# Optimization experiments

Measured on AMD Instinct MI355X. Metric: run time of the kernel, lower is better.

## Reference

```python
import jax, jax.numpy as jnp
import numpy as np

H, KV, D, HID, FF = 32, 8, 128, 4096, 14336
EPS = 1e-5
ROPE_THETA = 1e9


def setup_inputs() -> dict:
    key = jax.random.key(0)
    ks = jax.random.split(key, 10)
    B, S = 1, 2048
    s = 0.02
    return {
        "hidden_states": jax.random.normal(ks[0], (B, S, HID), dtype=jnp.float32),
        "wq": jax.random.normal(ks[1], (HID, H * D), dtype=jnp.float32) * s,
        "wk": jax.random.normal(ks[2], (HID, KV * D), dtype=jnp.float32) * s,
        "wv": jax.random.normal(ks[3], (HID, KV * D), dtype=jnp.float32) * s,
        "wo": jax.random.normal(ks[4], (H * D, HID), dtype=jnp.float32) * s,
        "w_gate": jax.random.normal(ks[5], (HID, FF), dtype=jnp.float32) * s,
        "w_up": jax.random.normal(ks[6], (HID, FF), dtype=jnp.float32) * s,
        "w_down": jax.random.normal(ks[7], (FF, HID), dtype=jnp.float32) * s,
        "ln1_w": jnp.ones((HID,), dtype=jnp.float32),
        "ln2_w": jnp.ones((HID,), dtype=jnp.float32),
        "position_ids": jnp.arange(B * S, dtype=jnp.int32).reshape(B, S),
    }


def _rmsnorm(x, w):
    var = jnp.mean(jnp.square(x), axis=-1, keepdims=True)
    return x * jax.lax.rsqrt(var + EPS) * w


def _rope_cos_sin(position_ids):
    inv_freq = 1.0 / (ROPE_THETA ** (jnp.arange(0, D, 2, dtype=jnp.float32) / D))  # [D/2]
    ang = position_ids.astype(jnp.float32)[..., None] * inv_freq  # [B,S,D/2]
    ang = jnp.concatenate([ang, ang], axis=-1)  # [B,S,D]
    return jnp.cos(ang), jnp.sin(ang)


def _rotate_half(x):
    x1, x2 = x[..., : D // 2], x[..., D // 2:]
    return jnp.concatenate([-x2, x1], axis=-1)


def _apply_rope(x, cos, sin):
    # x: [B,S,h,D]; cos/sin: [B,S,D]
    c, s = cos[:, :, None, :], sin[:, :, None, :]
    return x * c + _rotate_half(x) * s


def reference(hidden_states, wq, wk, wv, wo, w_gate, w_up, w_down, ln1_w, ln2_w, position_ids):
    B, S, _ = hidden_states.shape
    G = H // KV  # query groups per kv head

    # --- attention block ---
    residual = hidden_states
    x = _rmsnorm(hidden_states, ln1_w)
    q = (x @ wq).reshape(B, S, H, D)
    k = (x @ wk).reshape(B, S, KV, D)
    v = (x @ wv).reshape(B, S, KV, D)

    cos, sin = _rope_cos_sin(position_ids)
    q = _apply_rope(q, cos, sin)
    k = _apply_rope(k, cos, sin)

    # GQA: group query heads over kv heads, [B,S,KV,G,D]
    qg = q.reshape(B, S, KV, G, D)
    scores = jnp.einsum("bqhgd,bkhd->bhgqk", qg, k) / jnp.sqrt(jnp.float32(D))
    causal = position_ids[:, :, None] >= position_ids[:, None, :]  # [B,S,S]
    scores = jnp.where(causal[:, None, None, :, :], scores, jnp.float32(-1e9))
    probs = jax.nn.softmax(scores, axis=-1)
    attn = jnp.einsum("bhgqk,bkhd->bqhgd", probs, v).reshape(B, S, H * D)
    hidden_states = residual + attn @ wo

    # --- MLP block (SwiGLU) ---
    residual = hidden_states
    x = _rmsnorm(hidden_states, ln2_w)
    mlp = (jax.nn.silu(x @ w_gate) * (x @ w_up)) @ w_down
    return residual + mlp
```

## Files before the change

kernel.cpp:

```cpp
#include <hip/hip_runtime.h>

typedef short bf16x8 __attribute__((ext_vector_type(8)));
typedef float f32x4 __attribute__((ext_vector_type(4)));

#define DEV __device__ __forceinline__

constexpr int SEQ = 2048;
constexpr int HID = 4096;
constexpr int NH  = 32;
constexpr int NKV = 8;
constexpr int DH  = 128;
constexpr int FF  = 14336;
constexpr int QKVN = NH * DH + 2 * NKV * DH;

DEV unsigned short f2bf(float f) {
  union { float f; unsigned u; } x; x.f = f;
  unsigned r = x.u + 0x7fffu + ((x.u >> 16) & 1u);
  return (unsigned short)(r >> 16);
}
DEV float bf2f(unsigned short u) {
  union { unsigned u; float f; } x; x.u = ((unsigned)u) << 16; return x.f;
}
DEV void gload16(const void* g, void* l) {
  __builtin_amdgcn_global_load_lds(
      (const __attribute__((address_space(1))) unsigned*)g,
      (__attribute__((address_space(3))) unsigned*)l, 16, 0, 0);
}

__global__ __launch_bounds__(256) void rmsnorm_kernel(
    const float* __restrict__ x, const float* __restrict__ w,
    unsigned short* __restrict__ out) {
  const int row = blockIdx.x;
  const int tid = threadIdx.x;
  const float* xr = x + (size_t)row * HID;
  float4 v[4];
  float ss = 0.f;
#pragma unroll
  for (int i = 0; i < 4; ++i) {
    v[i] = *(const float4*)(xr + i * 1024 + tid * 4);
    ss += v[i].x * v[i].x + v[i].y * v[i].y + v[i].z * v[i].z + v[i].w * v[i].w;
  }
#pragma unroll
  for (int m = 1; m < 64; m <<= 1) ss += __shfl_xor(ss, m);
  __shared__ float red[4];
  if ((tid & 63) == 0) red[tid >> 6] = ss;
  __syncthreads();
  float tot = red[0] + red[1] + red[2] + red[3];
  float rms = rsqrtf(tot / (float)HID + 1e-5f);
  unsigned short* orow = out + (size_t)row * HID;
#pragma unroll
  for (int i = 0; i < 4; ++i) {
    int base = i * 1024 + tid * 4;
    ushort4 o;
    o.x = f2bf(v[i].x * rms * w[base + 0]);
    o.y = f2bf(v[i].y * rms * w[base + 1]);
    o.z = f2bf(v[i].z * rms * w[base + 2]);
    o.w = f2bf(v[i].w * rms * w[base + 3]);
    *(ushort4*)(orow + base) = o;
  }
}

__global__ __launch_bounds__(256) void wtrans_kernel(
    const float* __restrict__ W, unsigned short* __restrict__ WT, int K,
    int N) {
  __shared__ unsigned short t[64][72];
  const int k0 = blockIdx.x * 64, n0 = blockIdx.y * 64;
  const int tid = threadIdx.x;
  const int tk = tid >> 4;
  const int tn4 = (tid & 15) * 4;
#pragma unroll
  for (int p = 0; p < 4; ++p) {
    int k = tk + p * 16;
    float4 v = *(const float4*)(W + (size_t)(k0 + k) * N + n0 + tn4);
    t[tn4 + 0][k] = f2bf(v.x);
    t[tn4 + 1][k] = f2bf(v.y);
    t[tn4 + 2][k] = f2bf(v.z);
    t[tn4 + 3][k] = f2bf(v.w);
  }
  __syncthreads();
#pragma unroll
  for (int p = 0; p < 4; ++p) {
    int n = tk + p * 16;
    ushort4 o = *(const ushort4*)&t[n][tn4];
    *(ushort4*)(WT + (size_t)(n0 + n) * K + k0 + tn4) = o;
  }
}

__global__ __launch_bounds__(256) void rope_kernel(unsigned short* __restrict__ x,
                                                   int nheads, int ld) {
  const int gid = blockIdx.x * 256 + threadIdx.x;
  const int i = gid & 63;
  const int t = gid >> 6;
  const int s = t / nheads;
  const int hh = t - s * nheads;
  float ang = (float)s * exp2f((float)i * (-29.897352853986263f / 64.f));
  float sn, cs;
  sincosf(ang, &sn, &cs);
  size_t base = (size_t)s * ld + hh * DH + i;
  float x1 = bf2f(x[base]);
  float x2 = bf2f(x[base + 64]);
  x[base]      = f2bf(x1 * cs - x2 * sn);
  x[base + 64] = f2bf(x2 * cs + x1 * sn);
}

__global__ __launch_bounds__(256) void silu_mul_kernel(
    const unsigned short* __restrict__ g, const unsigned short* __restrict__ u,
    unsigned short* __restrict__ out) {
  const size_t idx = ((size_t)blockIdx.x * 256 + threadIdx.x) * 4;
  ushort4 gv = *(const ushort4*)(g + idx);
  ushort4 uv = *(const ushort4*)(u + idx);
  float gf[4] = {bf2f(gv.x), bf2f(gv.y), bf2f(gv.z), bf2f(gv.w)};
  float uf[4] = {bf2f(uv.x), bf2f(uv.y), bf2f(uv.z), bf2f(uv.w)};
  ushort4 o;
  unsigned short* op = (unsigned short*)&o;
#pragma unroll
  for (int j = 0; j < 4; ++j) {
    float sl = gf[j] / (1.f + __expf(-gf[j]));
    op[j] = f2bf(sl * uf[j]);
  }
  *(ushort4*)(out + idx) = o;
}

__global__ __launch_bounds__(256) void combine_kernel(
    const float* __restrict__ p0, const float* __restrict__ p1,
    const float* __restrict__ res, float* __restrict__ out) {
  const size_t i = ((size_t)blockIdx.x * 256 + threadIdx.x) * 4;
  float4 a = *(const float4*)(p0 + i);
  float4 b = *(const float4*)(p1 + i);
  float4 c = *(const float4*)(res + i);
  float4 o;
  o.x = a.x + b.x + c.x;
  o.y = a.y + b.y + c.y;
  o.z = a.z + b.z + c.z;
  o.w = a.w + b.w + c.w;
  *(float4*)(out + i) = o;
}

template <int EPI>
__global__ __launch_bounds__(512, 2) void gemm8p_kernel(
    const unsigned short* __restrict__ A, const unsigned short* __restrict__ BT,
    void* __restrict__ Cv0, void* __restrict__ Cv1, int gridM, int N, int Kld,
    int nsplit) {
  constexpr int MF = 4;
  constexpr int ABYTES = 256 * 128;
  constexpr int BUFBYTES = ABYTES + 32768;
  __shared__ __align__(128) char sm[2 * BUFBYTES];

  const int tid  = threadIdx.x;
  const int lane = tid & 63;
  const int wv   = tid >> 6;
  const int nwg = gridDim.x;
  const int b = blockIdx.x;
  const int logical = (b & 7) * (nwg >> 3) + (b >> 3);
  const int ntiles = nwg / nsplit;
  const int s = logical / ntiles;
  const int r = logical - s * ntiles;
  const int m0 = (r % gridM) * 256;
  const int n0 = (r / gridM) * 256;
  const int Klen = Kld / nsplit;
  const int koff = s * Klen;
  const int wm = (wv >> 2) * 128;
  const int wn = (wv & 3) * 64;
  const int nt = Klen >> 6;

  const int srow = tid >> 3;
  const int scolb = (tid & 7) * 16;
  const int sldsbase = wv * 1024;

  auto stage = [&](int h, int t) {
    const int buf = t & 1;
    const int kt = koff + t * 64;
    char* ldsOp;
    const unsigned short* g;
    int grow0, rowBase;
    if (h < 2) {
      ldsOp = sm + buf * BUFBYTES + ABYTES; g = BT; grow0 = n0; rowBase = h * 128;
    } else {
      ldsOp = sm + buf * BUFBYTES;          g = A;  grow0 = m0; rowBase = (h - 2) * 128;
    }
#pragma unroll
    for (int rr = 0; rr < 2; ++rr) {
      int row = rowBase + rr * 64 + srow;
      const char* gp = (const char*)g + ((size_t)(grow0 + row) * Kld + kt) * 2 +
                       (scolb ^ ((row & 7) << 4));
      gload16(gp, ldsOp + rowBase * 128 + rr * 8192 + sldsbase);
    }
  };

  const int kb0 = (lane >> 4) * 16;
  const int lrow = lane & 15;
  auto ldA = [&](const char* sA, int mh, int mf, int ks) {
    int row = wm + mh * 64 + mf * 16 + lrow;
    return *(const bf16x8*)(sA + ((row * 128 + kb0 + ks * 64) ^ ((row & 7) << 4)));
  };
  auto ldB = [&](const char* sB, int j, int ks) {
    int col = wn + j * 16 + lrow;
    return *(const bf16x8*)(sB + ((col * 128 + kb0 + ks * 64) ^ ((col & 7) << 4)));
  };

  f32x4 acc[2 * MF][4] = {};

  stage(2, 0); stage(3, 0); stage(0, 0); stage(1, 0);
  if (nt > 1) {
    stage(0, 1); stage(1, 1);
    asm volatile("s_waitcnt vmcnt(4)" ::: "memory");
  } else {
    asm volatile("s_waitcnt vmcnt(0)" ::: "memory");
  }
  __builtin_amdgcn_s_barrier();

  for (int t = 0; t < nt; ++t) {
    const char* sA = sm + (t & 1) * BUFBYTES;
    const char* sB = sA + ABYTES;
    bf16x8 a[MF], bb[4][2];

#pragma unroll
    for (int j = 0; j < 4; ++j) bb[j][0] = ldB(sB, j, 0);
#pragma unroll
    for (int mf = 0; mf < MF; ++mf) a[mf] = ldA(sA, 0, mf, 0);
    if (t + 1 < nt) stage(2, t + 1);
    __builtin_amdgcn_sched_barrier(0);
    __builtin_amdgcn_s_barrier();
    __builtin_amdgcn_s_setprio(1);
#pragma unroll
    for (int mf = 0; mf < MF; ++mf)
#pragma unroll
      for (int j = 0; j < 4; ++j)
        acc[mf][j] = __builtin_amdgcn_mfma_f32_16x16x32_bf16(
            a[mf], bb[j][0], acc[mf][j], 0, 0, 0);
    __builtin_amdgcn_s_setprio(0);
    __builtin_amdgcn_sched_barrier(0);
    __builtin_amdgcn_s_barrier();

#pragma unroll
    for (int j = 0; j < 4; ++j) bb[j][1] = ldB(sB, j, 1);
#pragma unroll
    for (int mf = 0; mf < MF; ++mf) a[mf] = ldA(sA, 0, mf, 1);
    if (t + 1 < nt) stage(3, t + 1);
    __builtin_amdgcn_sched_barrier(0);
    __builtin_amdgcn_s_barrier();
    __builtin_amdgcn_s_setprio(1);
#pragma unroll
    for (int mf = 0; mf < MF; ++mf)
#pragma unroll
      for (int j = 0; j < 4; ++j)
        acc[mf][j] = __builtin_amdgcn_mfma_f32_16x16x32_bf16(
            a[mf], bb[j][1], acc[mf][j], 0, 0, 0);
    __builtin_amdgcn_s_setprio(0);
    __builtin_amdgcn_sched_barrier(0);
    __builtin_amdgcn_s_barrier();

#pragma unroll
    for (int mf = 0; mf < MF; ++mf) a[mf] = ldA(sA, 1, mf, 0);
    if (t + 2 < nt) stage(0, t + 2);
    __builtin_amdgcn_sched_barrier(0);
    __builtin_amdgcn_s_barrier();
    __builtin_amdgcn_s_setprio(1);
#pragma unroll
    for (int mf = 0; mf < MF; ++mf)
#pragma unroll
      for (int j = 0; j < 4; ++j)
        acc[MF + mf][j] = __builtin_amdgcn_mfma_f32_16x16x32_bf16(
            a[mf], bb[j][0], acc[MF + mf][j], 0, 0, 0);
    __builtin_amdgcn_s_setprio(0);
    __builtin_amdgcn_sched_barrier(0);
    __builtin_amdgcn_s_barrier();

#pragma unroll
    for (int mf = 0; mf < MF; ++mf) a[mf] = ldA(sA, 1, mf, 1);
    if (t + 2 < nt) {
      stage(1, t + 2);
      asm volatile("s_waitcnt vmcnt(4)" ::: "memory");
    } else {
      asm volatile("s_waitcnt vmcnt(0)" ::: "memory");
    }
    __builtin_amdgcn_sched_barrier(0);
    __builtin_amdgcn_s_barrier();
    __builtin_amdgcn_s_setprio(1);
#pragma unroll
    for (int mf = 0; mf < MF; ++mf)
#pragma unroll
      for (int j = 0; j < 4; ++j)
        acc[MF + mf][j] = __builtin_amdgcn_mfma_f32_16x16x32_bf16(
            a[mf], bb[j][1], acc[MF + mf][j], 0, 0, 0);
    __builtin_amdgcn_s_setprio(0);
    __builtin_amdgcn_sched_barrier(0);
    __builtin_amdgcn_s_barrier();
  }

  const int rb = (lane >> 4) * 4;
  float* P = (float*)(s ? Cv1 : Cv0);
#pragma unroll
  for (int i = 0; i < 2 * MF; ++i) {
    const int mh = i / MF, mf = i % MF;
#pragma unroll
    for (int j = 0; j < 4; ++j) {
#pragma unroll
      for (int rr = 0; rr < 4; ++rr) {
        size_t row = (size_t)(m0 + wm + mh * 64 + mf * 16 + rb + rr);
        size_t col = (size_t)(n0 + wn + j * 16 + lrow);
        float vv = acc[i][j][rr];
        if (EPI == 0) {
          ((unsigned short*)Cv0)[row * N + col] = f2bf(vv);
        } else {
          P[row * N + col] = vv;
        }
      }
    }
  }
}

__global__ __launch_bounds__(512, 1) void attn_kernel(
    const unsigned short* __restrict__ QKV, unsigned short* __restrict__ Ob) {
  __shared__ __align__(128) char sm[114688];
  char* sQ  = sm;
  char* sK0 = sm + 32768;
  char* sK1 = sm + 49152;
  char* sV0 = sm + 65536;
  char* sV1 = sm + 81920;
  char* sP  = sm + 98304;
  const int tid  = threadIdx.x;
  const int lane = tid & 63;
  const int wv   = tid >> 6;
  const int logical = blockIdx.x;
  const int xr = 15 - (logical >> 5);
  const int h = logical & 31;
  const int qb0 = xr * 128;
  const int hkv = h >> 2;
  const int rbase = (lane >> 4) * 4;
  const int cbase = lane & 15;
  const unsigned short* Qp = QKV + h * DH;
  const unsigned short* Kp = QKV + NH * DH + hkv * DH;
  const unsigned short* Vp = QKV + NH * DH + NKV * DH + hkv * DH;

#pragma unroll
  for (int i = 0; i < 4; ++i) {
    int offs = i * 8192 + tid * 16;
    int row = offs >> 8, col = offs & 255;
    const char* gp = (const char*)Qp + ((size_t)(qb0 + row) * QKVN) * 2 +
                     (col ^ ((row & 15) << 4));
    gload16(gp, sQ + i * 8192 + wv * 1024);
  }

  auto stageK = [&](int t) {
    char* dst = (t & 1) ? sK1 : sK0;
    const int kt0 = t * 64;
#pragma unroll
    for (int i = 0; i < 2; ++i) {
      int offs = i * 8192 + tid * 16;
      int row = offs >> 8, col = offs & 255;
      const char* gp = (const char*)Kp + ((size_t)(kt0 + row) * QKVN) * 2 +
                       (col ^ ((row & 15) << 4));
      gload16(gp, dst + i * 8192 + wv * 1024);
    }
  };

  const int d4  = (tid & 31) * 4;
  const int kv4 = (tid >> 5) * 4;
  const int rot = (tid >> 1) & 3;
  auto loadV = [&](int t, ushort4* vr) {
    const unsigned short* g0 = Vp + (size_t)(t * 64 + kv4) * QKVN + d4;
#pragma unroll
    for (int k = 0; k < 4; ++k) vr[k] = *(const ushort4*)(g0 + (size_t)k * QKVN);
  };
  auto writeV = [&](int t, const ushort4* vr) {
    char* dst = (t & 1) ? sV1 : sV0;
    const unsigned short* a0 = (const unsigned short*)&vr[0];
    const unsigned short* a1 = (const unsigned short*)&vr[1];
    const unsigned short* a2 = (const unsigned short*)&vr[2];
    const unsigned short* a3 = (const unsigned short*)&vr[3];
#pragma unroll
    for (int j = 0; j < 4; ++j) {
      int jj = (j + rot) & 3;
      int dd = d4 + jj;
      uint2 pk;
      pk.x = (unsigned)a0[jj] | ((unsigned)a1[jj] << 16);
      pk.y = (unsigned)a2[jj] | ((unsigned)a3[jj] << 16);
      *(uint2*)(dst + ((dd * 128 + kv4 * 2) ^ ((dd & 7) << 4))) = pk;
    }
  };

  ushort4 vr[4];
  stageK(0);
  loadV(0, vr);
  asm volatile("s_waitcnt vmcnt(0)" ::: "memory");
  writeV(0, vr);
  __syncthreads();

  const int qrow = wv * 16 + (lane & 15);
  bf16x8 aq[4];
#pragma unroll
  for (int kk = 0; kk < 4; ++kk) {
    int kb = (lane >> 4) * 16 + kk * 64;
    aq[kk] = *(const bf16x8*)(sQ + ((qrow * 256 + kb) ^ ((qrow & 15) << 4)));
  }

  f32x4 oacc[8] = {};
  float m_r[4] = {-1e30f, -1e30f, -1e30f, -1e30f};
  float l_r[4] = {0.f, 0.f, 0.f, 0.f};
  const int ntiles = 2 * (xr + 1);

  for (int t = 0; t < ntiles; ++t) {
    const int kt0 = t * 64;
    const char* cK = (t & 1) ? sK1 : sK0;
    const char* cV = (t & 1) ? sV1 : sV0;
    if (t + 1 < ntiles) {
      stageK(t + 1);
      loadV(t + 1, vr);
    }

    f32x4 sacc[4] = {};
#pragma unroll
    for (int kk = 0; kk < 4; ++kk) {
      int kb = (lane >> 4) * 16 + kk * 64;
#pragma unroll
      for (int ni = 0; ni < 4; ++ni) {
        int krow = ni * 16 + (lane & 15);
        bf16x8 bk =
            *(const bf16x8*)(cK + ((krow * 256 + kb) ^ ((krow & 15) << 4)));
        sacc[ni] = __builtin_amdgcn_mfma_f32_16x16x32_bf16(aq[kk], bk,
                                                           sacc[ni], 0, 0, 0);
      }
    }

    const float scale = 0.08838834764831845f;
#pragma unroll
    for (int r = 0; r < 4; ++r) {
      int qg = qb0 + wv * 16 + rbase + r;
      float mx = -1e30f;
#pragma unroll
      for (int ni = 0; ni < 4; ++ni) {
        int cg = kt0 + ni * 16 + cbase;
        float sv = sacc[ni][r] * scale;
        sv = (cg <= qg) ? sv : -1e30f;
        sacc[ni][r] = sv;
        mx = fmaxf(mx, sv);
      }
      mx = fmaxf(mx, __shfl_xor(mx, 1));
      mx = fmaxf(mx, __shfl_xor(mx, 2));
      mx = fmaxf(mx, __shfl_xor(mx, 4));
      mx = fmaxf(mx, __shfl_xor(mx, 8));
      float mnew = fmaxf(m_r[r], mx);
      float sf = __expf(m_r[r] - mnew);
      m_r[r] = mnew;
      float rsum = 0.f;
#pragma unroll
      for (int ni = 0; ni < 4; ++ni) {
        float pv = __expf(sacc[ni][r] - mnew);
        sacc[ni][r] = pv;
        rsum += pv;
      }
      rsum += __shfl_xor(rsum, 1);
      rsum += __shfl_xor(rsum, 2);
      rsum += __shfl_xor(rsum, 4);
      rsum += __shfl_xor(rsum, 8);
      l_r[r] = l_r[r] * sf + rsum;
#pragma unroll
      for (int nt2 = 0; nt2 < 8; ++nt2) oacc[nt2][r] *= sf;
    }

    char* pw = sP + wv * 2048;
#pragma unroll
    for (int ni = 0; ni < 4; ++ni)
#pragma unroll
      for (int r = 0; r < 4; ++r) {
        int row = rbase + r;
        int cb2 = (ni * 16 + cbase) * 2;
        *(unsigned short*)(pw + ((row * 128 + cb2) ^ ((row & 7) << 4))) =
            f2bf(sacc[ni][r]);
      }
    asm volatile("s_waitcnt lgkmcnt(0)" ::: "memory");

#pragma unroll
    for (int kk = 0; kk < 2; ++kk) {
      int kb = (lane >> 4) * 16 + kk * 64;
      int prow = lane & 15;
      bf16x8 ap =
          *(const bf16x8*)(pw + ((prow * 128 + kb) ^ ((prow & 7) << 4)));
#pragma unroll
      for (int nt2 = 0; nt2 < 8; ++nt2) {
        int vrow = nt2 * 16 + (lane & 15);
        bf16x8 bv =
            *(const bf16x8*)(cV + ((vrow * 128 + kb) ^ ((vrow & 7) << 4)));
        oacc[nt2] =
            __builtin_amdgcn_mfma_f32_16x16x32_bf16(ap, bv, oacc[nt2], 0, 0, 0);
      }
    }

    if (t + 1 < ntiles) {
      asm volatile("s_waitcnt vmcnt(0)" ::: "memory");
      writeV(t + 1, vr);
    }
    __syncthreads();
  }

#pragma unroll
  for (int nt2 = 0; nt2 < 8; ++nt2)
#pragma unroll
    for (int r = 0; r < 4; ++r) {
      size_t row = (size_t)(qb0 + wv * 16 + rbase + r);
      int col = nt2 * 16 + cbase;
      Ob[row * (NH * DH) + h * DH + col] = f2bf(oacc[nt2][r] / l_r[r]);
    }
}

extern "C" void kernel_launch(void* const* d_in, const int* in_sizes, int n_in,
                              void* d_out, int out_size, void* d_ws,
                              size_t ws_size, hipStream_t stream) {
  const float* hs  = (const float*)d_in[0];
  const float* wq  = (const float*)d_in[1];
  const float* wk  = (const float*)d_in[2];
  const float* wvp = (const float*)d_in[3];
  const float* wo  = (const float*)d_in[4];
  const float* wg  = (const float*)d_in[5];
  const float* wu  = (const float*)d_in[6];
  const float* wd  = (const float*)d_in[7];
  const float* ln1 = (const float*)d_in[8];
  const float* ln2 = (const float*)d_in[9];

  char* p = (char*)d_ws;
  size_t need = 0;
  auto alloc = [&](size_t bytes) {
    char* r = p + need;
    need += (bytes + 255) & ~(size_t)255;
    return r;
  };
  unsigned short* T1   = (unsigned short*)alloc((size_t)FF * HID * 2);
  unsigned short* xn   = (unsigned short*)alloc((size_t)SEQ * HID * 2);
  unsigned short* qkv  = (unsigned short*)alloc((size_t)SEQ * QKVN * 2);
  unsigned short* ab   = (unsigned short*)alloc((size_t)SEQ * NH * DH * 2);
  float*          h2   = (float*)alloc((size_t)SEQ * HID * 4);
  unsigned short* xn2  = (unsigned short*)alloc((size_t)SEQ * HID * 2);
  unsigned short* gbuf = (unsigned short*)alloc((size_t)SEQ * FF * 2);
  unsigned short* ubuf = (unsigned short*)alloc((size_t)SEQ * FF * 2);
  if (need > ws_size) return;

  float* pO0 = (float*)gbuf;
  float* pO1 = (float*)ubuf;
  float* pD0 = (float*)ubuf;
  float* pD1 = (float*)xn;

  rmsnorm_kernel<<<SEQ, 256, 0, stream>>>(hs, ln1, xn);
  wtrans_kernel<<<dim3(HID / 64, HID / 64), 256, 0, stream>>>(wq, T1, HID, HID);
  wtrans_kernel<<<dim3(HID / 64, (NKV * DH) / 64), 256, 0, stream>>>(
      wk, T1 + (size_t)(NH * DH) * HID, HID, NKV * DH);
  wtrans_kernel<<<dim3(HID / 64, (NKV * DH) / 64), 256, 0, stream>>>(
      wvp, T1 + (size_t)(NH * DH + NKV * DH) * HID, HID, NKV * DH);
  gemm8p_kernel<0><<<(SEQ / 256) * (QKVN / 256), 512, 0, stream>>>(
      xn, T1, qkv, nullptr, SEQ / 256, QKVN, HID, 1);
  rope_kernel<<<(SEQ * NH * 64) / 256, 256, 0, stream>>>(qkv, NH, QKVN);
  rope_kernel<<<(SEQ * NKV * 64) / 256, 256, 0, stream>>>(qkv + NH * DH, NKV,
                                                          QKVN);
  attn_kernel<<<512, 512, 0, stream>>>(qkv, ab);
  wtrans_kernel<<<dim3(HID / 64, HID / 64), 256, 0, stream>>>(wo, T1, HID, HID);
  gemm8p_kernel<2><<<(SEQ / 256) * (HID / 256) * 2, 512, 0, stream>>>(
      ab, T1, pO0, pO1, SEQ / 256, HID, HID, 2);
  combine_kernel<<<(SEQ * HID) / 1024, 256, 0, stream>>>(pO0, pO1, hs, h2);
  rmsnorm_kernel<<<SEQ, 256, 0, stream>>>(h2, ln2, xn2);
  wtrans_kernel<<<dim3(HID / 64, FF / 64), 256, 0, stream>>>(wg, T1, HID, FF);
  gemm8p_kernel<0><<<(SEQ / 256) * (FF / 256), 512, 0, stream>>>(
      xn2, T1, gbuf, nullptr, SEQ / 256, FF, HID, 1);
  wtrans_kernel<<<dim3(HID / 64, FF / 64), 256, 0, stream>>>(wu, T1, HID, FF);
  gemm8p_kernel<0><<<(SEQ / 256) * (FF / 256), 512, 0, stream>>>(
      xn2, T1, ubuf, nullptr, SEQ / 256, FF, HID, 1);
  silu_mul_kernel<<<((size_t)SEQ * FF) / 1024, 256, 0, stream>>>(gbuf, ubuf,
                                                                 gbuf);
  wtrans_kernel<<<dim3(FF / 64, HID / 64), 256, 0, stream>>>(wd, T1, FF, HID);
  gemm8p_kernel<2><<<(SEQ / 256) * (HID / 256) * 2, 512, 0, stream>>>(
      gbuf, T1, pD0, pD1, SEQ / 256, HID, FF, 2);
  combine_kernel<<<(SEQ * HID) / 1024, 256, 0, stream>>>(pD0, pD1, h2,
                                                         (float*)d_out);
}
```

Measured before the change: 1.318 ms.

## Overlap weight transposes with GEMMs, fuse SiLU-mul into up GEMM and combine with RMSNorm

Adds extra workgroups to the GEMM kernel that transpose and convert the next weight matrix into a second buffer while the GEMM tiles run, so the Wo, Wup and Wdown transposes overlap compute instead of running as separate launches. The SiLU-multiply is fused into the up-projection epilogue, which reads the gate output in place and removes the ubuf round trip and the separate elementwise kernel. The attention-output combine is fused with the second RMSNorm. This path needs a larger workspace (the fat path) and falls back to the serial schedule otherwise. The transpose blocks compete with GEMM blocks for CUs and bandwidth, and the gate-input read in the epilogue adds uncoalesced loads.

```diff
diff --git a/kernel.cpp b/kernel.cpp
--- a/kernel.cpp
+++ b/kernel.cpp
@@ -103,24 +103,6 @@
   x[base + 64] = f2bf(x2 * cs + x1 * sn);
 }
 
-__global__ __launch_bounds__(256) void silu_mul_kernel(
-    const unsigned short* __restrict__ g, const unsigned short* __restrict__ u,
-    unsigned short* __restrict__ out) {
-  const size_t idx = ((size_t)blockIdx.x * 256 + threadIdx.x) * 4;
-  ushort4 gv = *(const ushort4*)(g + idx);
-  ushort4 uv = *(const ushort4*)(u + idx);
-  float gf[4] = {bf2f(gv.x), bf2f(gv.y), bf2f(gv.z), bf2f(gv.w)};
-  float uf[4] = {bf2f(uv.x), bf2f(uv.y), bf2f(uv.z), bf2f(uv.w)};
-  ushort4 o;
-  unsigned short* op = (unsigned short*)&o;
-#pragma unroll
-  for (int j = 0; j < 4; ++j) {
-    float sl = gf[j] / (1.f + __expf(-gf[j]));
-    op[j] = f2bf(sl * uf[j]);
-  }
-  *(ushort4*)(out + idx) = o;
-}
-
 __global__ __launch_bounds__(256) void combine_kernel(
     const float* __restrict__ p0, const float* __restrict__ p1,
     const float* __restrict__ res, float* __restrict__ out) {
@@ -136,20 +118,95 @@
   *(float4*)(out + i) = o;
 }
 
+__global__ __launch_bounds__(256) void combine_rms_kernel(
+    const float* __restrict__ p0, const float* __restrict__ p1,
+    const float* __restrict__ res, const float* __restrict__ w,
+    float* __restrict__ h2, unsigned short* __restrict__ xn2) {
+  const int row = blockIdx.x;
+  const int tid = threadIdx.x;
+  const size_t base = (size_t)row * HID;
+  float4 h[4];
+  float ss = 0.f;
+#pragma unroll
+  for (int i = 0; i < 4; ++i) {
+    size_t idx = base + i * 1024 + tid * 4;
+    float4 a = *(const float4*)(p0 + idx);
+    float4 b = *(const float4*)(p1 + idx);
+    float4 c = *(const float4*)(res + idx);
+    h[i].x = a.x + b.x + c.x;
+    h[i].y = a.y + b.y + c.y;
+    h[i].z = a.z + b.z + c.z;
+    h[i].w = a.w + b.w + c.w;
+    *(float4*)(h2 + idx) = h[i];
+    ss += h[i].x * h[i].x + h[i].y * h[i].y + h[i].z * h[i].z + h[i].w * h[i].w;
+  }
+#pragma unroll
+  for (int m = 1; m < 64; m <<= 1) ss += __shfl_xor(ss, m);
+  __shared__ float red[4];
+  if ((tid & 63) == 0) red[tid >> 6] = ss;
+  __syncthreads();
+  float tot = red[0] + red[1] + red[2] + red[3];
+  float rms = rsqrtf(tot / (float)HID + 1e-5f);
+#pragma unroll
+  for (int i = 0; i < 4; ++i) {
+    int off = i * 1024 + tid * 4;
+    ushort4 o;
+    o.x = f2bf(h[i].x * rms * w[off + 0]);
+    o.y = f2bf(h[i].y * rms * w[off + 1]);
+    o.z = f2bf(h[i].z * rms * w[off + 2]);
+    o.w = f2bf(h[i].w * rms * w[off + 3]);
+    *(ushort4*)(xn2 + base + off) = o;
+  }
+}
+
 template <int EPI>
 __global__ __launch_bounds__(512, 2) void gemm8p_kernel(
     const unsigned short* __restrict__ A, const unsigned short* __restrict__ BT,
     void* __restrict__ Cv0, void* __restrict__ Cv1, int gridM, int N, int Kld,
-    int nsplit) {
+    int nsplit, const float* __restrict__ TW, unsigned short* __restrict__ TWT,
+    int TK, int TN, int n_t) {
   constexpr int MF = 4;
   constexpr int ABYTES = 256 * 128;
   constexpr int BUFBYTES = ABYTES + 32768;
   __shared__ __align__(128) char sm[2 * BUFBYTES];
 
-  const int tid  = threadIdx.x;
+  const int tid = threadIdx.x;
+  const int nwg = gridDim.x - n_t;
+
+  if ((int)blockIdx.x >= nwg) {
+    const int team = tid >> 8, lt = tid & 255;
+    unsigned short(*tt)[72] = (unsigned short(*)[72])(sm + team * 9216);
+    const int tilesK = TK >> 6;
+    const int tot = tilesK * (TN >> 6);
+    const int tk = lt >> 4;
+    const int tn4 = (lt & 15) * 4;
+    for (int tile = ((int)blockIdx.x - nwg) * 2 + team; tile < tot;
+         tile += n_t * 2) {
+      const int k0 = (tile % tilesK) << 6;
+      const int n0t = (tile / tilesK) << 6;
+#pragma unroll
+      for (int p = 0; p < 4; ++p) {
+        int k = tk + p * 16;
+        float4 v = *(const float4*)(TW + (size_t)(k0 + k) * TN + n0t + tn4);
+        tt[tn4 + 0][k] = f2bf(v.x);
+        tt[tn4 + 1][k] = f2bf(v.y);
+        tt[tn4 + 2][k] = f2bf(v.z);
+        tt[tn4 + 3][k] = f2bf(v.w);
+      }
+      __syncthreads();
+#pragma unroll
+      for (int p = 0; p < 4; ++p) {
+        int n = tk + p * 16;
+        ushort4 o = *(const ushort4*)&tt[n][tn4];
+        *(ushort4*)(TWT + (size_t)(n0t + n) * TK + k0 + tn4) = o;
+      }
+      __syncthreads();
+    }
+    return;
+  }
+
   const int lane = tid & 63;
   const int wv   = tid >> 6;
-  const int nwg = gridDim.x;
   const int b = blockIdx.x;
   const int logical = (b & 7) * (nwg >> 3) + (b >> 3);
   const int ntiles = nwg / nsplit;
@@ -302,8 +359,12 @@
         float vv = acc[i][j][rr];
         if (EPI == 0) {
           ((unsigned short*)Cv0)[row * N + col] = f2bf(vv);
+        } else if (EPI == 2) {
+          P[row * N + col] = vv;
         } else {
-          P[row * N + col] = vv;
+          float g = bf2f(((const unsigned short*)Cv1)[row * N + col]);
+          float sl = g / (1.f + __expf(-g));
+          ((unsigned short*)Cv0)[row * N + col] = f2bf(sl * vv);
         }
       }
     }
@@ -533,12 +594,16 @@
   unsigned short* xn2  = (unsigned short*)alloc((size_t)SEQ * HID * 2);
   unsigned short* gbuf = (unsigned short*)alloc((size_t)SEQ * FF * 2);
   unsigned short* ubuf = (unsigned short*)alloc((size_t)SEQ * FF * 2);
-  if (need > ws_size) return;
+  size_t need_base = need;
+  unsigned short* T2   = (unsigned short*)alloc((size_t)FF * HID * 2);
+  const bool fat = (ws_size >= need);
+  if (ws_size < need_base) return;
 
   float* pO0 = (float*)gbuf;
-  float* pO1 = (float*)ubuf;
-  float* pD0 = (float*)ubuf;
-  float* pD1 = (float*)xn;
+  float* pO1 = (float*)xn;
+  float* pD0 = fat ? (float*)T2 : (float*)ubuf;
+  float* pD1 = fat ? (float*)(T2 + (size_t)SEQ * HID * 2) : (float*)xn;
+  (void)ubuf;
 
   rmsnorm_kernel<<<SEQ, 256, 0, stream>>>(hs, ln1, xn);
   wtrans_kernel<<<dim3(HID / 64, HID / 64), 256, 0, stream>>>(wq, T1, HID, HID);
@@ -546,28 +611,43 @@
       wk, T1 + (size_t)(NH * DH) * HID, HID, NKV * DH);
   wtrans_kernel<<<dim3(HID / 64, (NKV * DH) / 64), 256, 0, stream>>>(
       wvp, T1 + (size_t)(NH * DH + NKV * DH) * HID, HID, NKV * DH);
-  gemm8p_kernel<0><<<(SEQ / 256) * (QKVN / 256), 512, 0, stream>>>(
-      xn, T1, qkv, nullptr, SEQ / 256, QKVN, HID, 1);
+  if (fat) {
+    gemm8p_kernel<0><<<192 + 64, 512, 0, stream>>>(
+        xn, T1, qkv, nullptr, SEQ / 256, QKVN, HID, 1, wo, T2, HID, HID, 64);
+  } else {
+    gemm8p_kernel<0><<<192, 512, 0, stream>>>(
+        xn, T1, qkv, nullptr, SEQ / 256, QKVN, HID, 1, nullptr, nullptr, 64, 64, 0);
+  }
   rope_kernel<<<(SEQ * NH * 64) / 256, 256, 0, stream>>>(qkv, NH, QKVN);
   rope_kernel<<<(SEQ * NKV * 64) / 256, 256, 0, stream>>>(qkv + NH * DH, NKV,
                                                           QKVN);
   attn_kernel<<<512, 512, 0, stream>>>(qkv, ab);
-  wtrans_kernel<<<dim3(HID / 64, HID / 64), 256, 0, stream>>>(wo, T1, HID, HID);
-  gemm8p_kernel<2><<<(SEQ / 256) * (HID / 256) * 2, 512, 0, stream>>>(
-      ab, T1, pO0, pO1, SEQ / 256, HID, HID, 2);
-  combine_kernel<<<(SEQ * HID) / 1024, 256, 0, stream>>>(pO0, pO1, hs, h2);
-  rmsnorm_kernel<<<SEQ, 256, 0, stream>>>(h2, ln2, xn2);
+  unsigned short* Wo = fat ? T2 : T1;
+  if (!fat)
+    wtrans_kernel<<<dim3(HID / 64, HID / 64), 256, 0, stream>>>(wo, T1, HID, HID);
+  gemm8p_kernel<2><<<256, 512, 0, stream>>>(
+      ab, Wo, pO0, pO1, SEQ / 256, HID, HID, 2, nullptr, nullptr, 64, 64, 0);
+  combine_rms_kernel<<<SEQ, 256, 0, stream>>>(pO0, pO1, hs, ln2, h2, xn2);
   wtrans_kernel<<<dim3(HID / 64, FF / 64), 256, 0, stream>>>(wg, T1, HID, FF);
-  gemm8p_kernel<0><<<(SEQ / 256) * (FF / 256), 512, 0, stream>>>(
-      xn2, T1, gbuf, nullptr, SEQ / 256, FF, HID, 1);
-  wtrans_kernel<<<dim3(HID / 64, FF / 64), 256, 0, stream>>>(wu, T1, HID, FF);
-  gemm8p_kernel<0><<<(SEQ / 256) * (FF / 256), 512, 0, stream>>>(
-      xn2, T1, ubuf, nullptr, SEQ / 256, FF, HID, 1);
-  silu_mul_kernel<<<((size_t)SEQ * FF) / 1024, 256, 0, stream>>>(gbuf, ubuf,
-                                                                 gbuf);
-  wtrans_kernel<<<dim3(FF / 64, HID / 64), 256, 0, stream>>>(wd, T1, FF, HID);
-  gemm8p_kernel<2><<<(SEQ / 256) * (HID / 256) * 2, 512, 0, stream>>>(
-      gbuf, T1, pD0, pD1, SEQ / 256, HID, FF, 2);
+  if (fat) {
+    gemm8p_kernel<0><<<448 + 1024, 512, 0, stream>>>(
+        xn2, T1, gbuf, nullptr, SEQ / 256, FF, HID, 1, wu, T2, HID, FF, 1024);
+  } else {
+    gemm8p_kernel<0><<<448, 512, 0, stream>>>(
+        xn2, T1, gbuf, nullptr, SEQ / 256, FF, HID, 1, nullptr, nullptr, 64, 64, 0);
+  }
+  if (fat) {
+    gemm8p_kernel<3><<<448 + 1024, 512, 0, stream>>>(
+        xn2, T2, gbuf, gbuf, SEQ / 256, FF, HID, 1, wd, T1, FF, HID, 1024);
+  } else {
+    wtrans_kernel<<<dim3(HID / 64, FF / 64), 256, 0, stream>>>(wu, T1, HID, FF);
+    gemm8p_kernel<3><<<448, 512, 0, stream>>>(
+        xn2, T1, gbuf, gbuf, SEQ / 256, FF, HID, 1, nullptr, nullptr, 64, 64, 0);
+  }
+  if (!fat)
+    wtrans_kernel<<<dim3(FF / 64, HID / 64), 256, 0, stream>>>(wd, T1, FF, HID);
+  gemm8p_kernel<2><<<256, 512, 0, stream>>>(
+      gbuf, T1, pD0, pD1, SEQ / 256, HID, FF, 2, nullptr, nullptr, 64, 64, 0);
   combine_kernel<<<(SEQ * HID) / 1024, 256, 0, stream>>>(pD0, pD1, h2,
                                                          (float*)d_out);
 }
```

After: 1.227 ms. 1.07x faster.

## Fuse weight transpose/convert into GEMM B-load and fuse SiLU and RMSNorm epilogues

Applied to the files above, without the earlier changes.

Removes the separate fp32→bf16 weight-transpose kernels. The GEMM now reads the fp32 weights directly from global memory, converts them in registers and writes them into swizzled LDS, with the QKV GEMM selecting among wq/wk/wv per tile. It also folds the SiLU*up multiply into the up-projection epilogue, which reads gate from gbuf, and merges combine+rmsnorm into one kernel. This saves the weight-transpose passes and intermediate traffic. In exchange it adds register pressure, uncoalesced-ish scalar fp32 B loads (each lane strided by row), and a shallower one-ahead prefetch with full vmcnt(0) waits inside the K loop.

```diff
diff --git a/kernel.cpp b/kernel.cpp
--- a/kernel.cpp
+++ b/kernel.cpp
@@ -57,32 +57,6 @@
     o.z = f2bf(v[i].z * rms * w[base + 2]);
     o.w = f2bf(v[i].w * rms * w[base + 3]);
     *(ushort4*)(orow + base) = o;
-  }
-}
-
-__global__ __launch_bounds__(256) void wtrans_kernel(
-    const float* __restrict__ W, unsigned short* __restrict__ WT, int K,
-    int N) {
-  __shared__ unsigned short t[64][72];
-  const int k0 = blockIdx.x * 64, n0 = blockIdx.y * 64;
-  const int tid = threadIdx.x;
-  const int tk = tid >> 4;
-  const int tn4 = (tid & 15) * 4;
-#pragma unroll
-  for (int p = 0; p < 4; ++p) {
-    int k = tk + p * 16;
-    float4 v = *(const float4*)(W + (size_t)(k0 + k) * N + n0 + tn4);
-    t[tn4 + 0][k] = f2bf(v.x);
-    t[tn4 + 1][k] = f2bf(v.y);
-    t[tn4 + 2][k] = f2bf(v.z);
-    t[tn4 + 3][k] = f2bf(v.w);
-  }
-  __syncthreads();
-#pragma unroll
-  for (int p = 0; p < 4; ++p) {
-    int n = tk + p * 16;
-    ushort4 o = *(const ushort4*)&t[n][tn4];
-    *(ushort4*)(WT + (size_t)(n0 + n) * K + k0 + tn4) = o;
   }
 }
 
@@ -103,24 +77,6 @@
   x[base + 64] = f2bf(x2 * cs + x1 * sn);
 }
 
-__global__ __launch_bounds__(256) void silu_mul_kernel(
-    const unsigned short* __restrict__ g, const unsigned short* __restrict__ u,
-    unsigned short* __restrict__ out) {
-  const size_t idx = ((size_t)blockIdx.x * 256 + threadIdx.x) * 4;
-  ushort4 gv = *(const ushort4*)(g + idx);
-  ushort4 uv = *(const ushort4*)(u + idx);
-  float gf[4] = {bf2f(gv.x), bf2f(gv.y), bf2f(gv.z), bf2f(gv.w)};
-  float uf[4] = {bf2f(uv.x), bf2f(uv.y), bf2f(uv.z), bf2f(uv.w)};
-  ushort4 o;
-  unsigned short* op = (unsigned short*)&o;
-#pragma unroll
-  for (int j = 0; j < 4; ++j) {
-    float sl = gf[j] / (1.f + __expf(-gf[j]));
-    op[j] = f2bf(sl * uf[j]);
-  }
-  *(ushort4*)(out + idx) = o;
-}
-
 __global__ __launch_bounds__(256) void combine_kernel(
     const float* __restrict__ p0, const float* __restrict__ p1,
     const float* __restrict__ res, float* __restrict__ out) {
@@ -136,9 +92,51 @@
   *(float4*)(out + i) = o;
 }
 
-template <int EPI>
-__global__ __launch_bounds__(512, 2) void gemm8p_kernel(
-    const unsigned short* __restrict__ A, const unsigned short* __restrict__ BT,
+__global__ __launch_bounds__(256) void combine_rms_kernel(
+    const float* __restrict__ p0, const float* __restrict__ p1,
+    const float* __restrict__ res, const float* __restrict__ w,
+    float* __restrict__ h2, unsigned short* __restrict__ xn2) {
+  const int row = blockIdx.x;
+  const int tid = threadIdx.x;
+  const size_t base = (size_t)row * HID;
+  float4 h[4];
+  float ss = 0.f;
+#pragma unroll
+  for (int i = 0; i < 4; ++i) {
+    size_t idx = base + i * 1024 + tid * 4;
+    float4 a = *(const float4*)(p0 + idx);
+    float4 b = *(const float4*)(p1 + idx);
+    float4 c = *(const float4*)(res + idx);
+    h[i].x = a.x + b.x + c.x;
+    h[i].y = a.y + b.y + c.y;
+    h[i].z = a.z + b.z + c.z;
+    h[i].w = a.w + b.w + c.w;
+    *(float4*)(h2 + idx) = h[i];
+    ss += h[i].x * h[i].x + h[i].y * h[i].y + h[i].z * h[i].z + h[i].w * h[i].w;
+  }
+#pragma unroll
+  for (int m = 1; m < 64; m <<= 1) ss += __shfl_xor(ss, m);
+  __shared__ float red[4];
+  if ((tid & 63) == 0) red[tid >> 6] = ss;
+  __syncthreads();
+  float tot = red[0] + red[1] + red[2] + red[3];
+  float rms = rsqrtf(tot / (float)HID + 1e-5f);
+#pragma unroll
+  for (int i = 0; i < 4; ++i) {
+    int off = i * 1024 + tid * 4;
+    ushort4 o;
+    o.x = f2bf(h[i].x * rms * w[off + 0]);
+    o.y = f2bf(h[i].y * rms * w[off + 1]);
+    o.z = f2bf(h[i].z * rms * w[off + 2]);
+    o.w = f2bf(h[i].w * rms * w[off + 3]);
+    *(ushort4*)(xn2 + base + off) = o;
+  }
+}
+
+template <int EPI, int QKVSEL>
+__global__ __launch_bounds__(512, 2) void gemmF_kernel(
+    const unsigned short* __restrict__ A, const float* __restrict__ W0,
+    const float* __restrict__ W1, const float* __restrict__ W2,
     void* __restrict__ Cv0, void* __restrict__ Cv1, int gridM, int N, int Kld,
     int nsplit) {
   constexpr int MF = 4;
@@ -163,28 +161,54 @@
   const int wn = (wv & 3) * 64;
   const int nt = Klen >> 6;
 
+  const float* Bp;
+  int Nw, bn0;
+  if (QKVSEL) {
+    if (n0 < 4096)      { Bp = W0; Nw = 4096; bn0 = n0; }
+    else if (n0 < 5120) { Bp = W1; Nw = 1024; bn0 = n0 - 4096; }
+    else                { Bp = W2; Nw = 1024; bn0 = n0 - 5120; }
+  } else {
+    Bp = W0; Nw = N; bn0 = n0;
+  }
+
   const int srow = tid >> 3;
   const int scolb = (tid & 7) * 16;
   const int sldsbase = wv * 1024;
-
-  auto stage = [&](int h, int t) {
-    const int buf = t & 1;
+  auto stageA = [&](int half, int t) {
+    char* ldsOp = sm + ((t & 1) * BUFBYTES);
     const int kt = koff + t * 64;
-    char* ldsOp;
-    const unsigned short* g;
-    int grow0, rowBase;
-    if (h < 2) {
-      ldsOp = sm + buf * BUFBYTES + ABYTES; g = BT; grow0 = n0; rowBase = h * 128;
-    } else {
-      ldsOp = sm + buf * BUFBYTES;          g = A;  grow0 = m0; rowBase = (h - 2) * 128;
-    }
+    const int rowBase = half * 128;
 #pragma unroll
     for (int rr = 0; rr < 2; ++rr) {
       int row = rowBase + rr * 64 + srow;
-      const char* gp = (const char*)g + ((size_t)(grow0 + row) * Kld + kt) * 2 +
+      const char* gp = (const char*)A + ((size_t)(m0 + row) * Kld + kt) * 2 +
                        (scolb ^ ((row & 7) << 4));
       gload16(gp, ldsOp + rowBase * 128 + rr * 8192 + sldsbase);
     }
+  };
+
+  float bv[2][4][4];
+  auto loadBq = [&](int q, int t) {
+    const float* Wb = Bp + (size_t)(koff + t * 64 + wv * 8 + q * 4) * Nw +
+                      bn0 + lane;
+#pragma unroll
+    for (int j = 0; j < 4; ++j)
+#pragma unroll
+      for (int ki = 0; ki < 4; ++ki)
+        bv[q][j][ki] = Wb[(size_t)ki * Nw + 64 * j];
+  };
+  auto writeB = [&](char* sBw) {
+#pragma unroll
+    for (int q = 0; q < 2; ++q)
+#pragma unroll
+      for (int j = 0; j < 4; ++j) {
+        int n = 64 * j + lane;
+        int kq = wv * 8 + q * 4;
+        uint2 pk;
+        pk.x = (unsigned)f2bf(bv[q][j][0]) | ((unsigned)f2bf(bv[q][j][1]) << 16);
+        pk.y = (unsigned)f2bf(bv[q][j][2]) | ((unsigned)f2bf(bv[q][j][3]) << 16);
+        *(uint2*)(sBw + ((n * 128 + kq * 2) ^ ((n & 7) << 4))) = pk;
+      }
   };
 
   const int kb0 = (lane >> 4) * 16;
@@ -200,25 +224,28 @@
 
   f32x4 acc[2 * MF][4] = {};
 
-  stage(2, 0); stage(3, 0); stage(0, 0); stage(1, 0);
-  if (nt > 1) {
-    stage(0, 1); stage(1, 1);
-    asm volatile("s_waitcnt vmcnt(4)" ::: "memory");
-  } else {
-    asm volatile("s_waitcnt vmcnt(0)" ::: "memory");
-  }
+  loadBq(0, 0);
+  loadBq(1, 0);
+  stageA(0, 0);
+  stageA(1, 0);
+  asm volatile("s_waitcnt vmcnt(0)" ::: "memory");
+  writeB(sm + ABYTES);
+  asm volatile("s_waitcnt lgkmcnt(0)" ::: "memory");
+  __builtin_amdgcn_sched_barrier(0);
   __builtin_amdgcn_s_barrier();
 
   for (int t = 0; t < nt; ++t) {
     const char* sA = sm + (t & 1) * BUFBYTES;
     const char* sB = sA + ABYTES;
+    char* sBw = sm + (((t & 1) ^ 1) * BUFBYTES) + ABYTES;
+    const bool pf = (t + 1 < nt);
     bf16x8 a[MF], bb[4][2];
 
 #pragma unroll
     for (int j = 0; j < 4; ++j) bb[j][0] = ldB(sB, j, 0);
 #pragma unroll
     for (int mf = 0; mf < MF; ++mf) a[mf] = ldA(sA, 0, mf, 0);
-    if (t + 1 < nt) stage(2, t + 1);
+    if (pf) { loadBq(0, t + 1); stageA(0, t + 1); }
     __builtin_amdgcn_sched_barrier(0);
     __builtin_amdgcn_s_barrier();
     __builtin_amdgcn_s_setprio(1);
@@ -236,7 +263,7 @@
     for (int j = 0; j < 4; ++j) bb[j][1] = ldB(sB, j, 1);
 #pragma unroll
     for (int mf = 0; mf < MF; ++mf) a[mf] = ldA(sA, 0, mf, 1);
-    if (t + 1 < nt) stage(3, t + 1);
+    if (pf) { loadBq(1, t + 1); stageA(1, t + 1); }
     __builtin_amdgcn_sched_barrier(0);
     __builtin_amdgcn_s_barrier();
     __builtin_amdgcn_s_setprio(1);
@@ -252,7 +279,6 @@
 
 #pragma unroll
     for (int mf = 0; mf < MF; ++mf) a[mf] = ldA(sA, 1, mf, 0);
-    if (t + 2 < nt) stage(0, t + 2);
     __builtin_amdgcn_sched_barrier(0);
     __builtin_amdgcn_s_barrier();
     __builtin_amdgcn_s_setprio(1);
@@ -268,12 +294,9 @@
 
 #pragma unroll
     for (int mf = 0; mf < MF; ++mf) a[mf] = ldA(sA, 1, mf, 1);
-    if (t + 2 < nt) {
-      stage(1, t + 2);
-      asm volatile("s_waitcnt vmcnt(4)" ::: "memory");
-    } else {
-      asm volatile("s_waitcnt vmcnt(0)" ::: "memory");
-    }
+    asm volatile("s_waitcnt vmcnt(0)" ::: "memory");
+    if (pf) writeB(sBw);
+    asm volatile("s_waitcnt lgkmcnt(0)" ::: "memory");
     __builtin_amdgcn_sched_barrier(0);
     __builtin_amdgcn_s_barrier();
     __builtin_amdgcn_s_setprio(1);
@@ -302,8 +325,12 @@
         float vv = acc[i][j][rr];
         if (EPI == 0) {
           ((unsigned short*)Cv0)[row * N + col] = f2bf(vv);
+        } else if (EPI == 2) {
+          P[row * N + col] = vv;
         } else {
-          P[row * N + col] = vv;
+          float g = bf2f(((const unsigned short*)Cv1)[row * N + col]);
+          float sl = g / (1.f + __expf(-g));
+          ((unsigned short*)Cv0)[row * N + col] = f2bf(sl * vv);
         }
       }
     }
@@ -480,10 +507,10 @@
 #pragma unroll
       for (int nt2 = 0; nt2 < 8; ++nt2) {
         int vrow = nt2 * 16 + (lane & 15);
-        bf16x8 bv =
+        bf16x8 bv2 =
             *(const bf16x8*)(cV + ((vrow * 128 + kb) ^ ((vrow & 7) << 4)));
         oacc[nt2] =
-            __builtin_amdgcn_mfma_f32_16x16x32_bf16(ap, bv, oacc[nt2], 0, 0, 0);
+            __builtin_amdgcn_mfma_f32_16x16x32_bf16(ap, bv2, oacc[nt2], 0, 0, 0);
       }
     }
 
@@ -525,49 +552,32 @@
     need += (bytes + 255) & ~(size_t)255;
     return r;
   };
-  unsigned short* T1   = (unsigned short*)alloc((size_t)FF * HID * 2);
   unsigned short* xn   = (unsigned short*)alloc((size_t)SEQ * HID * 2);
   unsigned short* qkv  = (unsigned short*)alloc((size_t)SEQ * QKVN * 2);
   unsigned short* ab   = (unsigned short*)alloc((size_t)SEQ * NH * DH * 2);
   float*          h2   = (float*)alloc((size_t)SEQ * HID * 4);
   unsigned short* xn2  = (unsigned short*)alloc((size_t)SEQ * HID * 2);
   unsigned short* gbuf = (unsigned short*)alloc((size_t)SEQ * FF * 2);
-  unsigned short* ubuf = (unsigned short*)alloc((size_t)SEQ * FF * 2);
+  float*          pA   = (float*)alloc((size_t)SEQ * HID * 4);
+  float*          pB   = (float*)alloc((size_t)SEQ * HID * 4);
   if (need > ws_size) return;
 
-  float* pO0 = (float*)gbuf;
-  float* pO1 = (float*)ubuf;
-  float* pD0 = (float*)ubuf;
-  float* pD1 = (float*)xn;
-
   rmsnorm_kernel<<<SEQ, 256, 0, stream>>>(hs, ln1, xn);
-  wtrans_kernel<<<dim3(HID / 64, HID / 64), 256, 0, stream>>>(wq, T1, HID, HID);
-  wtrans_kernel<<<dim3(HID / 64, (NKV * DH) / 64), 256, 0, stream>>>(
-      wk, T1 + (size_t)(NH * DH) * HID, HID, NKV * DH);
-  wtrans_kernel<<<dim3(HID / 64, (NKV * DH) / 64), 256, 0, stream>>>(
-      wvp, T1 + (size_t)(NH * DH + NKV * DH) * HID, HID, NKV * DH);
-  gemm8p_kernel<0><<<(SEQ / 256) * (QKVN / 256), 512, 0, stream>>>(
-      xn, T1, qkv, nullptr, SEQ / 256, QKVN, HID, 1);
+  gemmF_kernel<0, 1><<<(SEQ / 256) * (QKVN / 256), 512, 0, stream>>>(
+      xn, wq, wk, wvp, qkv, nullptr, SEQ / 256, QKVN, HID, 1);
   rope_kernel<<<(SEQ * NH * 64) / 256, 256, 0, stream>>>(qkv, NH, QKVN);
   rope_kernel<<<(SEQ * NKV * 64) / 256, 256, 0, stream>>>(qkv + NH * DH, NKV,
                                                           QKVN);
   attn_kernel<<<512, 512, 0, stream>>>(qkv, ab);
-  wtrans_kernel<<<dim3(HID / 64, HID / 64), 256, 0, stream>>>(wo, T1, HID, HID);
-  gemm8p_kernel<2><<<(SEQ / 256) * (HID / 256) * 2, 512, 0, stream>>>(
-      ab, T1, pO0, pO1, SEQ / 256, HID, HID, 2);
-  combine_kernel<<<(SEQ * HID) / 1024, 256, 0, stream>>>(pO0, pO1, hs, h2);
-  rmsnorm_kernel<<<SEQ, 256, 0, stream>>>(h2, ln2, xn2);
-  wtrans_kernel<<<dim3(HID / 64, FF / 64), 256, 0, stream>>>(wg, T1, HID, FF);
-  gemm8p_kernel<0><<<(SEQ / 256) * (FF / 256), 512, 0, stream>>>(
-      xn2, T1, gbuf, nullptr, SEQ / 256, FF, HID, 1);
-  wtrans_kernel<<<dim3(HID / 64, FF / 64), 256, 0, stream>>>(wu, T1, HID, FF);
-  gemm8p_kernel<0><<<(SEQ / 256) * (FF / 256), 512, 0, stream>>>(
-      xn2, T1, ubuf, nullptr, SEQ / 256, FF, HID, 1);
-  silu_mul_kernel<<<((size_t)SEQ * FF) / 1024, 256, 0, stream>>>(gbuf, ubuf,
-                                                                 gbuf);
-  wtrans_kernel<<<dim3(FF / 64, HID / 64), 256, 0, stream>>>(wd, T1, FF, HID);
-  gemm8p_kernel<2><<<(SEQ / 256) * (HID / 256) * 2, 512, 0, stream>>>(
-      gbuf, T1, pD0, pD1, SEQ / 256, HID, FF, 2);
-  combine_kernel<<<(SEQ * HID) / 1024, 256, 0, stream>>>(pD0, pD1, h2,
+  gemmF_kernel<2, 0><<<256, 512, 0, stream>>>(ab, wo, nullptr, nullptr, pA, pB,
+                                              SEQ / 256, HID, HID, 2);
+  combine_rms_kernel<<<SEQ, 256, 0, stream>>>(pA, pB, hs, ln2, h2, xn2);
+  gemmF_kernel<0, 0><<<(SEQ / 256) * (FF / 256), 512, 0, stream>>>(
+      xn2, wg, nullptr, nullptr, gbuf, nullptr, SEQ / 256, FF, HID, 1);
+  gemmF_kernel<3, 0><<<(SEQ / 256) * (FF / 256), 512, 0, stream>>>(
+      xn2, wu, nullptr, nullptr, gbuf, gbuf, SEQ / 256, FF, HID, 1);
+  gemmF_kernel<2, 0><<<256, 512, 0, stream>>>(gbuf, wd, nullptr, nullptr, pA,
+                                              pB, SEQ / 256, HID, FF, 2);
+  combine_kernel<<<(SEQ * HID) / 1024, 256, 0, stream>>>(pA, pB, h2,
                                                          (float*)d_out);
 }
```

Result: slower. 1.885 ms (+43.1%).
